# Kernel tuning notes

Measured on AMD Instinct MI355X. Metric: run time of the kernel, lower is better.

Reference implementation:

```python
import jax, jax.numpy as jnp
import numpy as np

N_ITER = 2  # args.n_iter; aggregator = 'sum'


def setup_inputs() -> dict:
    key = jax.random.key(0)
    B, D, S = 8192, 128, 16
    NUM_USER, NUM_ENT, NUM_REL = 100000, 500000, 64
    ks = jax.random.split(key, 9)
    return {
        "u": jax.random.randint(ks[0], (B,), 0, NUM_USER),
        "v": jax.random.randint(ks[1], (B,), 0, NUM_ENT),
        "adj_ent": jax.random.randint(ks[2], (NUM_ENT, S), 0, NUM_ENT),
        "adj_rel": jax.random.randint(ks[3], (NUM_ENT, S), 0, NUM_REL),
        "usr_table": jax.random.normal(ks[4], (NUM_USER, D), jnp.float32) * 0.1,
        "ent_table": jax.random.normal(ks[5], (NUM_ENT, D), jnp.float32) * 0.1,
        "rel_table": jax.random.normal(ks[6], (NUM_REL, D), jnp.float32) * 0.1,
        "W": jax.random.normal(ks[7], (D, D), jnp.float32) * (1.0 / np.sqrt(D)),
        "b": jnp.zeros((D,), jnp.float32),
    }


def reference(u, v, adj_ent, adj_rel, usr_table, ent_table, rel_table, W, b):
    # NOTE: in the original code, _message_passing always reads base entity
    # embeddings for neighbors, so the neighbor message is identical at every
    # hop and the output depends only on v's own adjacency row.
    u_emb = usr_table[u]                              # [B, D]
    nbr_emb = ent_table[adj_ent[v]]                   # [B, S, D] gather
    rel_emb = rel_table[adj_rel[v]]                   # [B, S, D] gather
    scores = jnp.einsum('bd,bsd->bs', u_emb, rel_emb)  # pi_{u,r}
    attn = jax.nn.softmax(scores, axis=-1)            # softmax over S neighbors
    msg = jnp.einsum('bs,bsd->bd', attn, nbr_emb)     # weighted neighbor sum
    rep = ent_table[v]                                # rep^0 = ent(v)
    for _ in range(N_ITER):                           # 'sum' aggregator, eq.4
        rep = jax.nn.relu((msg + rep) @ W + b)
    return jax.nn.sigmoid(jnp.sum(u_emb * rep, axis=1))  # [B]
```

## Files before the change

### kernel.cpp

```cpp
#include <hip/hip_runtime.h>

#define D 128
#define S 16

__global__ __launch_bounds__(256) void kgcn_fused(
    const int* __restrict__ u, const int* __restrict__ v,
    const int* __restrict__ adj_ent, const int* __restrict__ adj_rel,
    const float* __restrict__ usr, const float* __restrict__ ent,
    const float* __restrict__ rel, const float* __restrict__ W,
    const float* __restrict__ bias, float* __restrict__ out)
{
    __shared__ float sX[8 * D];

    const int tid  = threadIdx.x;
    const int grp  = tid >> 5;
    const int lane = tid & 31;
    const int b    = blockIdx.x * 8 + grp;

    const int uu = u[b];
    const int vv = v[b];

    const float4 u4   = *(const float4*)(usr + (size_t)uu * D + lane * 4);
    const float4 rep0 = *(const float4*)(ent + (size_t)vv * D + lane * 4);

    const int ae = adj_ent[(size_t)vv * S + (lane & 15)];
    const int ar = adj_rel[(size_t)vv * S + (lane & 15)];

    float sc[S];
    float4 r4[8], n4a[8], n4b[8];

    #pragma unroll
    for (int s = 0; s < 8; ++s) {
        const int nr = __shfl(ar, s, 32);
        r4[s] = *(const float4*)(rel + (size_t)nr * D + lane * 4);
    }
    #pragma unroll
    for (int s = 0; s < 8; ++s) {
        const int ne = __shfl(ae, s, 32);
        n4a[s] = *(const float4*)(ent + (size_t)ne * D + lane * 4);
    }
    #pragma unroll
    for (int s = 0; s < 8; ++s) {
        float p = u4.x * r4[s].x + u4.y * r4[s].y +
                  u4.z * r4[s].z + u4.w * r4[s].w;
        #pragma unroll
        for (int off = 16; off >= 1; off >>= 1) p += __shfl_xor(p, off, 32);
        sc[s] = p;
    }
    #pragma unroll
    for (int s = 0; s < 8; ++s) {
        const int nr = __shfl(ar, 8 + s, 32);
        r4[s] = *(const float4*)(rel + (size_t)nr * D + lane * 4);
    }
    #pragma unroll
    for (int s = 0; s < 8; ++s) {
        float p = u4.x * r4[s].x + u4.y * r4[s].y +
                  u4.z * r4[s].z + u4.w * r4[s].w;
        #pragma unroll
        for (int off = 16; off >= 1; off >>= 1) p += __shfl_xor(p, off, 32);
        sc[8 + s] = p;
    }

    float mx = sc[0];
    #pragma unroll
    for (int s = 1; s < S; ++s) mx = fmaxf(mx, sc[s]);
    float sum = 0.f;
    #pragma unroll
    for (int s = 0; s < S; ++s) { sc[s] = __expf(sc[s] - mx); sum += sc[s]; }
    const float inv = 1.f / sum;

    #pragma unroll
    for (int s = 0; s < 8; ++s) {
        const int ne = __shfl(ae, 8 + s, 32);
        n4b[s] = *(const float4*)(ent + (size_t)ne * D + lane * 4);
    }

    float m0 = 0.f, m1 = 0.f, m2 = 0.f, m3 = 0.f;
    #pragma unroll
    for (int s = 0; s < 8; ++s) {
        const float a = sc[s] * inv;
        m0 += a * n4a[s].x; m1 += a * n4a[s].y;
        m2 += a * n4a[s].z; m3 += a * n4a[s].w;
    }
    #pragma unroll
    for (int s = 0; s < 8; ++s) {
        const float a = sc[8 + s] * inv;
        m0 += a * n4b[s].x; m1 += a * n4b[s].y;
        m2 += a * n4b[s].z; m3 += a * n4b[s].w;
    }

    const int j0 = lane * 4;
    const float4 b4 = *(const float4*)(bias + j0);
    const float* xrow = &sX[grp * D];

    *(float4*)&sX[grp * D + j0] =
        make_float4(m0 + rep0.x, m1 + rep0.y, m2 + rep0.z, m3 + rep0.w);
    __syncthreads();

    float4 y;
    {
        float a0 = 0.f, a1 = 0.f, a2 = 0.f, a3 = 0.f;
        #pragma unroll 4
        for (int d = 0; d < D; ++d) {
            const float4 w4 = *(const float4*)(W + d * D + j0);
            const float xm = xrow[d];
            a0 += xm * w4.x; a1 += xm * w4.y;
            a2 += xm * w4.z; a3 += xm * w4.w;
        }
        y.x = fmaxf(a0 + b4.x, 0.f);
        y.y = fmaxf(a1 + b4.y, 0.f);
        y.z = fmaxf(a2 + b4.z, 0.f);
        y.w = fmaxf(a3 + b4.w, 0.f);
    }
    __syncthreads();

    *(float4*)&sX[grp * D + j0] =
        make_float4(m0 + y.x, m1 + y.y, m2 + y.z, m3 + y.w);
    __syncthreads();

    {
        float a0 = 0.f, a1 = 0.f, a2 = 0.f, a3 = 0.f;
        #pragma unroll 4
        for (int d = 0; d < D; ++d) {
            const float4 w4 = *(const float4*)(W + d * D + j0);
            const float xm = xrow[d];
            a0 += xm * w4.x; a1 += xm * w4.y;
            a2 += xm * w4.z; a3 += xm * w4.w;
        }
        y.x = fmaxf(a0 + b4.x, 0.f);
        y.y = fmaxf(a1 + b4.y, 0.f);
        y.z = fmaxf(a2 + b4.z, 0.f);
        y.w = fmaxf(a3 + b4.w, 0.f);
    }

    float pr = u4.x * y.x + u4.y * y.y + u4.z * y.z + u4.w * y.w;
    #pragma unroll
    for (int off = 16; off >= 1; off >>= 1) pr += __shfl_xor(pr, off, 32);
    if (lane == 0) out[b] = 1.f / (1.f + __expf(-pr));
}

extern "C" void kernel_launch(void* const* d_in, const int* in_sizes, int n_in,
                              void* d_out, int out_size, void* d_ws, size_t ws_size,
                              hipStream_t stream)
{
    const int* u       = (const int*)d_in[0];
    const int* v       = (const int*)d_in[1];
    const int* adj_ent = (const int*)d_in[2];
    const int* adj_rel = (const int*)d_in[3];
    const float* usr   = (const float*)d_in[4];
    const float* ent   = (const float*)d_in[5];
    const float* rel   = (const float*)d_in[6];
    const float* W     = (const float*)d_in[7];
    const float* bias  = (const float*)d_in[8];
    float* out = (float*)d_out;

    hipLaunchKernelGGL(kgcn_fused, dim3(8192 / 8), dim3(256), 0, stream,
                       u, v, adj_ent, adj_rel, usr, ent, rel, W, bias, out);
}
```

Measured before the change: 386.2 us.

## Process 16 batch rows per block and register-tile the W matmul

Each block now handles 16 batch elements, and each 32-lane group gathers two elements serially in a non-unrolled loop. The two dense layers are recomputed as a register-blocked tile: each thread computes 4 rows by 2 output columns, so each W load is reused across 4 rows instead of 1. This is meant to cut per-row W reads and the serial per-column dot-product overhead. In exchange, the gathers for the two elements per group run one after the other, which halves gather parallelism per block, and the grid shrinks to 512 blocks.

```diff
diff --git a/kernel.cpp b/kernel.cpp
--- a/kernel.cpp
+++ b/kernel.cpp
@@ -10,133 +10,190 @@
     const float* __restrict__ rel, const float* __restrict__ W,
     const float* __restrict__ bias, float* __restrict__ out)
 {
-    __shared__ float sX[8 * D];
-
-    const int tid  = threadIdx.x;
-    const int grp  = tid >> 5;
-    const int lane = tid & 31;
-    const int b    = blockIdx.x * 8 + grp;
-
-    const int uu = u[b];
-    const int vv = v[b];
-
-    const float4 u4   = *(const float4*)(usr + (size_t)uu * D + lane * 4);
-    const float4 rep0 = *(const float4*)(ent + (size_t)vv * D + lane * 4);
-
-    const int ae = adj_ent[(size_t)vv * S + (lane & 15)];
-    const int ar = adj_rel[(size_t)vv * S + (lane & 15)];
-
-    float sc[S];
-    float4 r4[8], n4a[8], n4b[8];
+    __shared__ float sX[16 * D];
+    __shared__ float sMsg[16 * D];
+
+    const int tid = threadIdx.x;
+    const int g   = tid >> 5;
+    const int ln  = tid & 31;
+    const int b0  = blockIdx.x * 16;
+
+    float4 u4k[2];
+
+    #pragma unroll 1
+    for (int i = 0; i < 2; ++i) {
+        const int e  = g * 2 + i;
+        const int b  = b0 + e;
+        const int uu = u[b];
+        const int vv = v[b];
+
+        const float4 u4   = *(const float4*)(usr + (size_t)uu * D + ln * 4);
+        const float4 rep0 = *(const float4*)(ent + (size_t)vv * D + ln * 4);
+
+        const int ae = adj_ent[(size_t)vv * S + (ln & 15)];
+        const int ar = adj_rel[(size_t)vv * S + (ln & 15)];
+
+        float sc[S];
+        float4 r4[8], n4a[8], n4b[8];
+
+        #pragma unroll
+        for (int s = 0; s < 8; ++s) {
+            const int nr = __shfl(ar, s, 32);
+            r4[s] = *(const float4*)(rel + (size_t)nr * D + ln * 4);
+        }
+        #pragma unroll
+        for (int s = 0; s < 8; ++s) {
+            const int ne = __shfl(ae, s, 32);
+            n4a[s] = *(const float4*)(ent + (size_t)ne * D + ln * 4);
+        }
+        #pragma unroll
+        for (int s = 0; s < 8; ++s) {
+            float p = u4.x * r4[s].x + u4.y * r4[s].y +
+                      u4.z * r4[s].z + u4.w * r4[s].w;
+            #pragma unroll
+            for (int off = 16; off >= 1; off >>= 1) p += __shfl_xor(p, off, 32);
+            sc[s] = p;
+        }
+        #pragma unroll
+        for (int s = 0; s < 8; ++s) {
+            const int nr = __shfl(ar, 8 + s, 32);
+            r4[s] = *(const float4*)(rel + (size_t)nr * D + ln * 4);
+        }
+        #pragma unroll
+        for (int s = 0; s < 8; ++s) {
+            float p = u4.x * r4[s].x + u4.y * r4[s].y +
+                      u4.z * r4[s].z + u4.w * r4[s].w;
+            #pragma unroll
+            for (int off = 16; off >= 1; off >>= 1) p += __shfl_xor(p, off, 32);
+            sc[8 + s] = p;
+        }
+
+        float mx = sc[0];
+        #pragma unroll
+        for (int s = 1; s < S; ++s) mx = fmaxf(mx, sc[s]);
+        float sum = 0.f;
+        #pragma unroll
+        for (int s = 0; s < S; ++s) { sc[s] = __expf(sc[s] - mx); sum += sc[s]; }
+        const float inv = 1.f / sum;
+
+        #pragma unroll
+        for (int s = 0; s < 8; ++s) {
+            const int ne = __shfl(ae, 8 + s, 32);
+            n4b[s] = *(const float4*)(ent + (size_t)ne * D + ln * 4);
+        }
+
+        float m0 = 0.f, m1 = 0.f, m2 = 0.f, m3 = 0.f;
+        #pragma unroll
+        for (int s = 0; s < 8; ++s) {
+            const float a = sc[s] * inv;
+            m0 += a * n4a[s].x; m1 += a * n4a[s].y;
+            m2 += a * n4a[s].z; m3 += a * n4a[s].w;
+        }
+        #pragma unroll
+        for (int s = 0; s < 8; ++s) {
+            const float a = sc[8 + s] * inv;
+            m0 += a * n4b[s].x; m1 += a * n4b[s].y;
+            m2 += a * n4b[s].z; m3 += a * n4b[s].w;
+        }
+
+        *(float4*)&sMsg[e * D + ln * 4] = make_float4(m0, m1, m2, m3);
+        *(float4*)&sX[e * D + ln * 4] =
+            make_float4(m0 + rep0.x, m1 + rep0.y, m2 + rep0.z, m3 + rep0.w);
+        u4k[i] = u4;
+    }
+    __syncthreads();
+
+    const int gc  = g & 1;
+    const int gr  = g >> 1;
+    const int m0r = gr * 4;
+    const int j0  = gc * 64 + ln * 2;
+    const float2 b2 = *(const float2*)(bias + j0);
+
+    float y[4][2];
+
+    {
+        float acc[4][2];
+        #pragma unroll
+        for (int k = 0; k < 4; ++k) { acc[k][0] = 0.f; acc[k][1] = 0.f; }
+
+        #pragma unroll 4
+        for (int d0 = 0; d0 < D; d0 += 4) {
+            float4 xv[4];
+            #pragma unroll
+            for (int k = 0; k < 4; ++k)
+                xv[k] = *(const float4*)&sX[(m0r + k) * D + d0];
+            #pragma unroll
+            for (int dd = 0; dd < 4; ++dd) {
+                const float2 w2 = *(const float2*)(W + (d0 + dd) * D + j0);
+                #pragma unroll
+                for (int k = 0; k < 4; ++k) {
+                    const float xm = dd == 0 ? xv[k].x : dd == 1 ? xv[k].y
+                                   : dd == 2 ? xv[k].z : xv[k].w;
+                    acc[k][0] += xm * w2.x; acc[k][1] += xm * w2.y;
+                }
+            }
+        }
+        #pragma unroll
+        for (int k = 0; k < 4; ++k) {
+            y[k][0] = fmaxf(acc[k][0] + b2.x, 0.f);
+            y[k][1] = fmaxf(acc[k][1] + b2.y, 0.f);
+        }
+    }
+    __syncthreads();
 
     #pragma unroll
-    for (int s = 0; s < 8; ++s) {
-        const int nr = __shfl(ar, s, 32);
-        r4[s] = *(const float4*)(rel + (size_t)nr * D + lane * 4);
-    }
+    for (int k = 0; k < 4; ++k) {
+        const float2 mg2 = *(const float2*)&sMsg[(m0r + k) * D + j0];
+        *(float2*)&sX[(m0r + k) * D + j0] =
+            make_float2(mg2.x + y[k][0], mg2.y + y[k][1]);
+    }
+    __syncthreads();
+
+    {
+        float acc[4][2];
+        #pragma unroll
+        for (int k = 0; k < 4; ++k) { acc[k][0] = 0.f; acc[k][1] = 0.f; }
+
+        #pragma unroll 4
+        for (int d0 = 0; d0 < D; d0 += 4) {
+            float4 xv[4];
+            #pragma unroll
+            for (int k = 0; k < 4; ++k)
+                xv[k] = *(const float4*)&sX[(m0r + k) * D + d0];
+            #pragma unroll
+            for (int dd = 0; dd < 4; ++dd) {
+                const float2 w2 = *(const float2*)(W + (d0 + dd) * D + j0);
+                #pragma unroll
+                for (int k = 0; k < 4; ++k) {
+                    const float xm = dd == 0 ? xv[k].x : dd == 1 ? xv[k].y
+                                   : dd == 2 ? xv[k].z : xv[k].w;
+                    acc[k][0] += xm * w2.x; acc[k][1] += xm * w2.y;
+                }
+            }
+        }
+        #pragma unroll
+        for (int k = 0; k < 4; ++k) {
+            y[k][0] = fmaxf(acc[k][0] + b2.x, 0.f);
+            y[k][1] = fmaxf(acc[k][1] + b2.y, 0.f);
+        }
+    }
+    __syncthreads();
+
     #pragma unroll
-    for (int s = 0; s < 8; ++s) {
-        const int ne = __shfl(ae, s, 32);
-        n4a[s] = *(const float4*)(ent + (size_t)ne * D + lane * 4);
-    }
+    for (int k = 0; k < 4; ++k)
+        *(float2*)&sX[(m0r + k) * D + j0] = make_float2(y[k][0], y[k][1]);
+    __syncthreads();
+
     #pragma unroll
-    for (int s = 0; s < 8; ++s) {
-        float p = u4.x * r4[s].x + u4.y * r4[s].y +
-                  u4.z * r4[s].z + u4.w * r4[s].w;
-        #pragma unroll
-        for (int off = 16; off >= 1; off >>= 1) p += __shfl_xor(p, off, 32);
-        sc[s] = p;
-    }
-    #pragma unroll
-    for (int s = 0; s < 8; ++s) {
-        const int nr = __shfl(ar, 8 + s, 32);
-        r4[s] = *(const float4*)(rel + (size_t)nr * D + lane * 4);
-    }
-    #pragma unroll
-    for (int s = 0; s < 8; ++s) {
-        float p = u4.x * r4[s].x + u4.y * r4[s].y +
-                  u4.z * r4[s].z + u4.w * r4[s].w;
-        #pragma unroll
-        for (int off = 16; off >= 1; off >>= 1) p += __shfl_xor(p, off, 32);
-        sc[8 + s] = p;
-    }
-
-    float mx = sc[0];
-    #pragma unroll
-    for (int s = 1; s < S; ++s) mx = fmaxf(mx, sc[s]);
-    float sum = 0.f;
-    #pragma unroll
-    for (int s = 0; s < S; ++s) { sc[s] = __expf(sc[s] - mx); sum += sc[s]; }
-    const float inv = 1.f / sum;
-
-    #pragma unroll
-    for (int s = 0; s < 8; ++s) {
-        const int ne = __shfl(ae, 8 + s, 32);
-        n4b[s] = *(const float4*)(ent + (size_t)ne * D + lane * 4);
-    }
-
-    float m0 = 0.f, m1 = 0.f, m2 = 0.f, m3 = 0.f;
-    #pragma unroll
-    for (int s = 0; s < 8; ++s) {
-        const float a = sc[s] * inv;
-        m0 += a * n4a[s].x; m1 += a * n4a[s].y;
-        m2 += a * n4a[s].z; m3 += a * n4a[s].w;
-    }
-    #pragma unroll
-    for (int s = 0; s < 8; ++s) {
-        const float a = sc[8 + s] * inv;
-        m0 += a * n4b[s].x; m1 += a * n4b[s].y;
-        m2 += a * n4b[s].z; m3 += a * n4b[s].w;
-    }
-
-    const int j0 = lane * 4;
-    const float4 b4 = *(const float4*)(bias + j0);
-    const float* xrow = &sX[grp * D];
-
-    *(float4*)&sX[grp * D + j0] =
-        make_float4(m0 + rep0.x, m1 + rep0.y, m2 + rep0.z, m3 + rep0.w);
-    __syncthreads();
-
-    float4 y;
-    {
-        float a0 = 0.f, a1 = 0.f, a2 = 0.f, a3 = 0.f;
-        #pragma unroll 4
-        for (int d = 0; d < D; ++d) {
-            const float4 w4 = *(const float4*)(W + d * D + j0);
-            const float xm = xrow[d];
-            a0 += xm * w4.x; a1 += xm * w4.y;
-            a2 += xm * w4.z; a3 += xm * w4.w;
-        }
-        y.x = fmaxf(a0 + b4.x, 0.f);
-        y.y = fmaxf(a1 + b4.y, 0.f);
-        y.z = fmaxf(a2 + b4.z, 0.f);
-        y.w = fmaxf(a3 + b4.w, 0.f);
-    }
-    __syncthreads();
-
-    *(float4*)&sX[grp * D + j0] =
-        make_float4(m0 + y.x, m1 + y.y, m2 + y.z, m3 + y.w);
-    __syncthreads();
-
-    {
-        float a0 = 0.f, a1 = 0.f, a2 = 0.f, a3 = 0.f;
-        #pragma unroll 4
-        for (int d = 0; d < D; ++d) {
-            const float4 w4 = *(const float4*)(W + d * D + j0);
-            const float xm = xrow[d];
-            a0 += xm * w4.x; a1 += xm * w4.y;
-            a2 += xm * w4.z; a3 += xm * w4.w;
-        }
-        y.x = fmaxf(a0 + b4.x, 0.f);
-        y.y = fmaxf(a1 + b4.y, 0.f);
-        y.z = fmaxf(a2 + b4.z, 0.f);
-        y.w = fmaxf(a3 + b4.w, 0.f);
-    }
-
-    float pr = u4.x * y.x + u4.y * y.y + u4.z * y.z + u4.w * y.w;
-    #pragma unroll
-    for (int off = 16; off >= 1; off >>= 1) pr += __shfl_xor(pr, off, 32);
-    if (lane == 0) out[b] = 1.f / (1.f + __expf(-pr));
+    for (int i = 0; i < 2; ++i) {
+        const int e = g * 2 + i;
+        const float4 rf = *(const float4*)&sX[e * D + ln * 4];
+        const float4 uf = u4k[i];
+        float pr = uf.x * rf.x + uf.y * rf.y + uf.z * rf.z + uf.w * rf.w;
+        #pragma unroll
+        for (int off = 16; off >= 1; off >>= 1) pr += __shfl_xor(pr, off, 32);
+        if (ln == 0) out[b0 + e] = 1.f / (1.f + __expf(-pr));
+    }
 }
 
 extern "C" void kernel_launch(void* const* d_in, const int* in_sizes, int n_in,
@@ -154,6 +211,6 @@
     const float* bias  = (const float*)d_in[8];
     float* out = (float*)d_out;
 
-    hipLaunchKernelGGL(kgcn_fused, dim3(8192 / 8), dim3(256), 0, stream,
+    hipLaunchKernelGGL(kgcn_fused, dim3(8192 / 16), dim3(256), 0, stream,
                        u, v, adj_ent, adj_rel, usr, ent, rel, W, bias, out);
 }
```

After: 376.2 us. -2.6%, faster.
